# Kernel tuning notes

Measured on AMD Instinct MI355X. Metric: run time of the kernel, lower is better.

The kernel has to match this reference:

```python
import jax, jax.numpy as jnp
import numpy as np

MAX_KL = 11  # max kernel length among {7,9,11}

def setup_inputs() -> dict:
    key = jax.random.key(0)
    T, K, C = 2048, 10000, 10  # input_length, n_kernels, nr_classes
    rng = np.random.default_rng(0)
    # --- ROCKET random kernels (faithful to build_kernels) ---
    Ls = rng.choice(np.array([7, 9, 11]), size=K)                  # kernel lengths
    w = rng.normal(size=(K, MAX_KL)).astype(np.float32)
    tapmask = np.arange(MAX_KL)[None, :] < Ls[:, None]
    w = w * tapmask
    w = (w - tapmask * (w.sum(1, keepdims=True) / Ls[:, None])).astype(np.float32)  # mean-centered
    b = (1.0 - 2.0 * rng.random(K)).astype(np.float32)             # bias in (-1, 1]
    A = np.log2((T - 1) / (Ls - 1.0))
    dil = np.floor(2.0 ** (rng.random(K) * A)).astype(np.int32)    # dilation
    pad = (rng.random(K) <= 0.5).astype(np.int32)                  # padding 0 or 1
    # --- input series and classifier params ---
    x = jax.random.normal(key, (1, 1, T), dtype=jnp.float32)
    k1, _ = jax.random.split(jax.random.fold_in(key, 1))
    Wc = (jax.random.normal(k1, (2 * K, C), dtype=jnp.float32) * 0.01).astype(jnp.float32)
    bc = jnp.zeros((C,), dtype=jnp.float32)
    return {
        "x": x,
        "w": jnp.asarray(w), "b": jnp.asarray(b),
        "dil": jnp.asarray(dil), "pad": jnp.asarray(pad), "Ls": jnp.asarray(Ls, jnp.int32),
        "Wc": Wc, "bc": bc,
    }


def reference(x, w, b, dil, pad, Ls, Wc, bc):
    # x: [1,1,T]; w: [K,11] (zero-padded taps); b,dil,pad,Ls: [K]; Wc: [2K,C]; bc: [C]
    T = x.shape[-1]
    K = w.shape[0]
    xp = jnp.pad(x[0, 0], (1, 1))                  # [T+2] padded signal (covers padding=1)
    S = T + 2                                      # max possible output length
    s = jnp.arange(S)                              # output positions
    start = (1 - pad)[:, None]                     # [K,1] offset into padded signal
    # out[i,s] = b_i + sum_j w[i,j] * xp[start_i + s + dil_i*j]
    out = jnp.broadcast_to(b[:, None], (K, S))
    for j in range(MAX_KL):                        # fixed small tap loop
        idx = jnp.clip(start + s[None, :] + dil[:, None] * j, 0, T + 1)  # [K,S]
        out = out + w[:, j:j + 1] * xp[idx]
    out_len = T + 2 * pad - dil * (Ls - 1)         # [K] true conv output lengths
    valid = s[None, :] < out_len[:, None]          # [K,S]
    ppv = jnp.sum(jnp.where(valid & (out > 0), 1.0, 0.0), axis=1) / out_len.astype(out.dtype)
    mx = jnp.max(jnp.where(valid, out, -jnp.inf), axis=1)
    feats = jnp.concatenate([ppv, mx])             # [2K] (ppv block then max block)
    return jax.nn.softmax(feats @ Wc + bc, axis=-1)
```

## Files before the change

kernel.cpp:

```cpp
#include <hip/hip_runtime.h>
#include <math.h>

#define T_LEN 2048
#define KNUM 10000
#define MAXKL 11
#define BPK 8
#define NBLK (KNUM / BPK)
#define XOFF 3
#define XP_SZ 2064
#define NB2 40
#define CHUNK2 500
#define NCLS 10

template<int L>
__device__ __forceinline__ void conv_loop(const float* __restrict__ XP, int tid,
    int out_len, int s0, int d, const float* __restrict__ wr, float bias,
    int& cnt, float& mx)
{
    for (int s2 = tid * 2; s2 < out_len; s2 += 512) {
        const int base = XOFF + s0 + s2;
        float a0 = bias, a1 = bias;
#pragma unroll
        for (int j = 0; j < L; ++j) {
            const float* p = XP + base + j * d;
            const float p0 = p[0];
            const float p1 = p[1];
            a0 = fmaf(wr[j], p0, a0);
            a1 = fmaf(wr[j], p1, a1);
        }
        cnt += (a0 > 0.0f) ? 1 : 0;
        mx = fmaxf(mx, a0);
        if (s2 + 1 < out_len) {
            cnt += (a1 > 0.0f) ? 1 : 0;
            mx = fmaxf(mx, a1);
        }
    }
}

__global__ __launch_bounds__(256) void rocket_feats_kernel(
    const float* __restrict__ x, const float* __restrict__ w,
    const float* __restrict__ b, const int* __restrict__ dil,
    const int* __restrict__ pad, const int* __restrict__ Ls,
    float* __restrict__ feats)
{
    __shared__ float XP[XP_SZ];
    __shared__ float rmx[BPK][4];
    __shared__ int   rcnt[BPK][4];

    const int tid = threadIdx.x;

    {
        const float4* x4 = (const float4*)x;
        float4* XP4 = (float4*)XP;
#pragma unroll
        for (int it = 0; it < T_LEN / 4 / 256; ++it)
            XP4[1 + it * 256 + tid] = x4[it * 256 + tid];
        if (tid < 4) XP[tid] = 0.0f;
        else if (tid < 8) XP[2048 + tid] = 0.0f;
    }
    __syncthreads();

    const int k0 = blockIdx.x * BPK;
    for (int kk = 0; kk < BPK; ++kk) {
        const int k = k0 + kk;
        float wr[MAXKL];
#pragma unroll
        for (int j = 0; j < MAXKL; ++j) wr[j] = w[k * MAXKL + j];
        const float bias = b[k];
        const int d = dil[k];
        const int p = pad[k];
        const int L = Ls[k];
        const int out_len = T_LEN + 2 * p - d * (L - 1);
        const int s0 = 1 - p;

        int cnt = 0;
        float mx = -INFINITY;
        if (L == 7)       conv_loop<7>(XP, tid, out_len, s0, d, wr, bias, cnt, mx);
        else if (L == 9)  conv_loop<9>(XP, tid, out_len, s0, d, wr, bias, cnt, mx);
        else              conv_loop<11>(XP, tid, out_len, s0, d, wr, bias, cnt, mx);

#pragma unroll
        for (int off = 32; off > 0; off >>= 1) {
            cnt += __shfl_down(cnt, off);
            mx = fmaxf(mx, __shfl_down(mx, off));
        }
        const int wv = tid >> 6;
        if ((tid & 63) == 0) { rmx[kk][wv] = mx; rcnt[kk][wv] = cnt; }
        __syncthreads();
        if (tid == 0) {
            const float m = fmaxf(fmaxf(rmx[kk][0], rmx[kk][1]),
                                  fmaxf(rmx[kk][2], rmx[kk][3]));
            const int c = rcnt[kk][0] + rcnt[kk][1] + rcnt[kk][2] + rcnt[kk][3];
            feats[k]        = (float)c / (float)out_len;
            feats[KNUM + k] = m;
        }
    }
}

__global__ __launch_bounds__(256) void rocket_logits_kernel(
    const float* __restrict__ feats, const float* __restrict__ Wc,
    float* __restrict__ partials)
{
    float acc[NCLS];
#pragma unroll
    for (int c = 0; c < NCLS; ++c) acc[c] = 0.0f;

    const int fbeg = blockIdx.x * CHUNK2;
    const int fend = fbeg + CHUNK2;
    for (int f = fbeg + threadIdx.x; f < fend; f += 256) {
        const float v = feats[f];
        const float* __restrict__ wrow = Wc + (size_t)f * NCLS;
#pragma unroll
        for (int c = 0; c < NCLS; ++c)
            acc[c] = fmaf(v, wrow[c], acc[c]);
    }

#pragma unroll
    for (int c = 0; c < NCLS; ++c) {
#pragma unroll
        for (int off = 32; off > 0; off >>= 1)
            acc[c] += __shfl_down(acc[c], off);
    }
    __shared__ float lds[4][NCLS];
    const int wave = threadIdx.x >> 6;
    if ((threadIdx.x & 63) == 0) {
#pragma unroll
        for (int c = 0; c < NCLS; ++c) lds[wave][c] = acc[c];
    }
    __syncthreads();
    if (threadIdx.x == 0) {
#pragma unroll
        for (int c = 0; c < NCLS; ++c)
            partials[blockIdx.x * NCLS + c] =
                lds[0][c] + lds[1][c] + lds[2][c] + lds[3][c];
    }
}

__global__ __launch_bounds__(64) void rocket_softmax_kernel(
    const float* __restrict__ partials, const float* __restrict__ bc,
    float* __restrict__ out)
{
    __shared__ float lg[NCLS];
    const int t = threadIdx.x;
    if (t < NCLS) {
        float s = bc[t];
        for (int i = 0; i < NB2; ++i) s += partials[i * NCLS + t];
        lg[t] = s;
    }
    __syncthreads();
    if (t == 0) {
        float m = lg[0];
#pragma unroll
        for (int i = 1; i < NCLS; ++i) m = fmaxf(m, lg[i]);
        float e[NCLS];
        float se = 0.0f;
#pragma unroll
        for (int i = 0; i < NCLS; ++i) { e[i] = expf(lg[i] - m); se += e[i]; }
        const float inv = 1.0f / se;
#pragma unroll
        for (int i = 0; i < NCLS; ++i) out[i] = e[i] * inv;
    }
}

extern "C" void kernel_launch(void* const* d_in, const int* in_sizes, int n_in,
                              void* d_out, int out_size, void* d_ws, size_t ws_size,
                              hipStream_t stream) {
    const float* x   = (const float*)d_in[0];
    const float* w   = (const float*)d_in[1];
    const float* b   = (const float*)d_in[2];
    const int*   dil = (const int*)d_in[3];
    const int*   pad = (const int*)d_in[4];
    const int*   Ls  = (const int*)d_in[5];
    const float* Wc  = (const float*)d_in[6];
    const float* bc  = (const float*)d_in[7];
    float* out = (float*)d_out;

    float* feats    = (float*)d_ws;
    float* partials = feats + 2 * KNUM;

    rocket_feats_kernel<<<NBLK, 256, 0, stream>>>(x, w, b, dil, pad, Ls, feats);
    rocket_logits_kernel<<<NB2, 256, 0, stream>>>(feats, Wc, partials);
    rocket_softmax_kernel<<<1, 64, 0, stream>>>(partials, bc, out);
}
```

Measured before the change: 101.4 us.

## Fuse classifier matvec into feature kernel, drop separate logits launch

Each feature block now multiplies its 8 kernels' ppv/max features by the matching Wc rows and writes 10 partial logits, removing the feats buffer and the separate logits kernel. The softmax kernel now reduces 1250 partials in two stages, through groups in shared memory. This saves one kernel launch and a global round trip of the features. In exchange it adds a block-wide sync and a tail step to every feature block, plus a larger final reduction.

```diff
diff --git a/kernel.cpp b/kernel.cpp
--- a/kernel.cpp
+++ b/kernel.cpp
@@ -8,9 +8,9 @@
 #define NBLK (KNUM / BPK)
 #define XOFF 3
 #define XP_SZ 2064
-#define NB2 40
-#define CHUNK2 500
 #define NCLS 10
+#define RGRP 50
+#define NGRP (NBLK / RGRP)
 
 template<int L>
 __device__ __forceinline__ void conv_loop(const float* __restrict__ XP, int tid,
@@ -41,11 +41,14 @@
     const float* __restrict__ x, const float* __restrict__ w,
     const float* __restrict__ b, const int* __restrict__ dil,
     const int* __restrict__ pad, const int* __restrict__ Ls,
-    float* __restrict__ feats)
+    const float* __restrict__ Wc,
+    float* __restrict__ partials)
 {
     __shared__ float XP[XP_SZ];
     __shared__ float rmx[BPK][4];
     __shared__ int   rcnt[BPK][4];
+    __shared__ float pv[BPK];
+    __shared__ float mv[BPK];
 
     const int tid = threadIdx.x;
 
@@ -91,60 +94,45 @@
             const float m = fmaxf(fmaxf(rmx[kk][0], rmx[kk][1]),
                                   fmaxf(rmx[kk][2], rmx[kk][3]));
             const int c = rcnt[kk][0] + rcnt[kk][1] + rcnt[kk][2] + rcnt[kk][3];
-            feats[k]        = (float)c / (float)out_len;
-            feats[KNUM + k] = m;
+            pv[kk] = (float)c / (float)out_len;
+            mv[kk] = m;
         }
+    }
+    __syncthreads();
+
+    if (tid < NCLS) {
+        float acc = 0.0f;
+#pragma unroll
+        for (int kk = 0; kk < BPK; ++kk) {
+            const int k = k0 + kk;
+            acc = fmaf(pv[kk], Wc[(size_t)k * NCLS + tid], acc);
+            acc = fmaf(mv[kk], Wc[(size_t)(KNUM + k) * NCLS + tid], acc);
+        }
+        partials[blockIdx.x * NCLS + tid] = acc;
     }
 }
 
-__global__ __launch_bounds__(256) void rocket_logits_kernel(
-    const float* __restrict__ feats, const float* __restrict__ Wc,
-    float* __restrict__ partials)
-{
-    float acc[NCLS];
-#pragma unroll
-    for (int c = 0; c < NCLS; ++c) acc[c] = 0.0f;
-
-    const int fbeg = blockIdx.x * CHUNK2;
-    const int fend = fbeg + CHUNK2;
-    for (int f = fbeg + threadIdx.x; f < fend; f += 256) {
-        const float v = feats[f];
-        const float* __restrict__ wrow = Wc + (size_t)f * NCLS;
-#pragma unroll
-        for (int c = 0; c < NCLS; ++c)
-            acc[c] = fmaf(v, wrow[c], acc[c]);
-    }
-
-#pragma unroll
-    for (int c = 0; c < NCLS; ++c) {
-#pragma unroll
-        for (int off = 32; off > 0; off >>= 1)
-            acc[c] += __shfl_down(acc[c], off);
-    }
-    __shared__ float lds[4][NCLS];
-    const int wave = threadIdx.x >> 6;
-    if ((threadIdx.x & 63) == 0) {
-#pragma unroll
-        for (int c = 0; c < NCLS; ++c) lds[wave][c] = acc[c];
-    }
-    __syncthreads();
-    if (threadIdx.x == 0) {
-#pragma unroll
-        for (int c = 0; c < NCLS; ++c)
-            partials[blockIdx.x * NCLS + c] =
-                lds[0][c] + lds[1][c] + lds[2][c] + lds[3][c];
-    }
-}
-
-__global__ __launch_bounds__(64) void rocket_softmax_kernel(
+__global__ __launch_bounds__(256) void rocket_softmax_kernel(
     const float* __restrict__ partials, const float* __restrict__ bc,
     float* __restrict__ out)
 {
+    __shared__ float lds[NGRP][NCLS];
     __shared__ float lg[NCLS];
     const int t = threadIdx.x;
+
+    if (t < NGRP * NCLS) {
+        const int c = t % NCLS;
+        const int g = t / NCLS;
+        float s = 0.0f;
+        const float* p = partials + (size_t)g * RGRP * NCLS + c;
+        for (int i = 0; i < RGRP; ++i) s += p[i * NCLS];
+        lds[g][c] = s;
+    }
+    __syncthreads();
     if (t < NCLS) {
         float s = bc[t];
-        for (int i = 0; i < NB2; ++i) s += partials[i * NCLS + t];
+#pragma unroll
+        for (int g = 0; g < NGRP; ++g) s += lds[g][t];
         lg[t] = s;
     }
     __syncthreads();
@@ -175,10 +163,8 @@
     const float* bc  = (const float*)d_in[7];
     float* out = (float*)d_out;
 
-    float* feats    = (float*)d_ws;
-    float* partials = feats + 2 * KNUM;
+    float* partials = (float*)d_ws;
 
-    rocket_feats_kernel<<<NBLK, 256, 0, stream>>>(x, w, b, dil, pad, Ls, feats);
-    rocket_logits_kernel<<<NB2, 256, 0, stream>>>(feats, Wc, partials);
-    rocket_softmax_kernel<<<1, 64, 0, stream>>>(partials, bc, out);
+    rocket_feats_kernel<<<NBLK, 256, 0, stream>>>(x, w, b, dil, pad, Ls, Wc, partials);
+    rocket_softmax_kernel<<<1, 256, 0, stream>>>(partials, bc, out);
 }
```

New measurement: 100.7 us. No clear change (-0.8%).
